# Kernel tuning notes

Hardware: AMD Instinct MI355X
Metric: run time of the kernel (lower is better)

The kernel has to match this reference:

```python
import jax, jax.numpy as jnp
import numpy as np

DM = 512; NH = 8; EL = 3; FACTOR = 3; EPS = 1e-5

def layernorm(x, g, b):
    m = x.mean(-1, keepdims=True)
    v = x.var(-1, keepdims=True)
    return (x - m) / jnp.sqrt(v + EPS) * g + b

def pos_embed(L, d):
    pos = jnp.arange(L, dtype=jnp.float32)[:, None]
    div = jnp.exp(jnp.arange(0, d, 2, dtype=jnp.float32) * (-np.log(10000.0) / d))
    pe = jnp.zeros((L, d), jnp.float32)
    pe = pe.at[:, 0::2].set(jnp.sin(pos * div))
    pe = pe.at[:, 1::2].set(jnp.cos(pos * div))
    return pe

def circ_conv1d(x, w, b=None):
    # x: [B,L,Cin], w: [Cout,Cin,3]; torch Conv1d padding=1, padding_mode='circular'
    xp = jnp.concatenate([x[:, -1:], x, x[:, :1]], axis=1)
    y = jax.lax.conv_general_dilated(xp, w, (1,), 'VALID', dimension_numbers=('NWC', 'OIW', 'NWC'))
    return y if b is None else y + b

def prob_attention(q, k, v, rng):
    # q,k,v: [B,H,L,D] -- Informer ProbSparse attention (non-masked encoder case)
    B, H, L, D = q.shape
    LK = k.shape[2]
    U = min(int(FACTOR * np.ceil(np.log(LK))), LK)   # sampled keys per query
    u = min(int(FACTOR * np.ceil(np.log(L))), L)     # top queries kept
    idx = jax.random.randint(rng, (L, U), 0, LK)     # shared across B,H as in torch
    k_samp = k[:, :, idx]                            # [B,H,L,U,D]
    qk = jnp.einsum('bhld,bhlud->bhlu', q, k_samp)
    M = qk.max(-1) - qk.sum(-1) / LK                 # sparsity measure
    top = jax.lax.top_k(M, u)[1]                     # [B,H,u]
    q_red = jnp.take_along_axis(q, top[..., None], axis=2)
    scores = jnp.einsum('bhud,bhkd->bhuk', q_red, k) / jnp.sqrt(jnp.asarray(D, q.dtype))
    attn = jax.nn.softmax(scores, axis=-1)
    upd = jnp.einsum('bhuk,bhkd->bhud', attn, v)
    ctx = jnp.broadcast_to(v.mean(axis=2, keepdims=True), (B, H, L, D))
    bi = jnp.arange(B)[:, None, None]
    hi = jnp.arange(H)[None, :, None]
    return ctx.at[bi, hi, top].set(upd)

def encoder_layer(x, p, rng):
    Wq_, bq_, Wk_, bk_, Wv_, bv_, Wo_, bo_, w1, b1, w2, b2, g1, be1, g2, be2 = p
    B, L, _ = x.shape
    D = DM // NH
    q = (x @ Wq_.T + bq_).reshape(B, L, NH, D).transpose(0, 2, 1, 3)
    k = (x @ Wk_.T + bk_).reshape(B, L, NH, D).transpose(0, 2, 1, 3)
    v = (x @ Wv_.T + bv_).reshape(B, L, NH, D).transpose(0, 2, 1, 3)
    ctx = prob_attention(q, k, v, rng).transpose(0, 2, 1, 3).reshape(B, L, DM)
    x = x + (ctx @ Wo_.T + bo_)
    x = layernorm(x, g1, be1)
    y = jax.nn.gelu(x @ w1.T + b1, approximate=False)  # pointwise conv1 (k=1)
    y = y @ w2.T + b2                                   # pointwise conv2 (k=1)
    return layernorm(x + y, g2, be2)

def distil_layer(x, w, b, g, beta):
    y = circ_conv1d(x, w, b)                 # Conv1d k=3 circular
    mu = y.mean((0, 1))
    var = y.var((0, 1))                      # BatchNorm1d, training stats
    y = (y - mu) / jnp.sqrt(var + EPS) * g + beta
    y = jax.nn.elu(y)
    # MaxPool1d(kernel=3, stride=2, padding=1)
    return jax.lax.reduce_window(y, -jnp.inf, jax.lax.max, (1, 3, 1), (1, 2, 1), ((0, 0), (1, 1), (0, 0)))

def setup_inputs():
    key = jax.random.key(0)
    ks = jax.random.split(key, 12)
    B, S, CIN, COUT, DFF = 8, 2048, 7, 7, 2048
    r = lambda k, s: jax.random.normal(k, s, jnp.float32)
    return {
        'x_enc': r(ks[0], (B, S, CIN)),
        'tok_w': r(ks[1], (DM, CIN, 3)) * (2.0 / (CIN * 3)) ** 0.5,
        'Wq': r(ks[2], (EL, DM, DM)) * DM ** -0.5, 'bq': jnp.zeros((EL, DM)),
        'Wk': r(ks[3], (EL, DM, DM)) * DM ** -0.5, 'bk': jnp.zeros((EL, DM)),
        'Wv': r(ks[4], (EL, DM, DM)) * DM ** -0.5, 'bv': jnp.zeros((EL, DM)),
        'Wo': r(ks[5], (EL, DM, DM)) * DM ** -0.5, 'bo': jnp.zeros((EL, DM)),
        'conv1_w': r(ks[6], (EL, DFF, DM)) * DM ** -0.5, 'conv1_b': jnp.zeros((EL, DFF)),
        'conv2_w': r(ks[7], (EL, DM, DFF)) * DFF ** -0.5, 'conv2_b': jnp.zeros((EL, DM)),
        'ln1_g': jnp.ones((EL, DM)), 'ln1_b': jnp.zeros((EL, DM)),
        'ln2_g': jnp.ones((EL, DM)), 'ln2_b': jnp.zeros((EL, DM)),
        'dconv_w': r(ks[8], (EL - 1, DM, DM, 3)) * (DM * 3) ** -0.5, 'dconv_b': jnp.zeros((EL - 1, DM)),
        'bn_g': jnp.ones((EL - 1, DM)), 'bn_b': jnp.zeros((EL - 1, DM)),
        'lnf_g': jnp.ones((DM,)), 'lnf_b': jnp.zeros((DM,)),
        'end_w': r(ks[9], (COUT, DM)) * DM ** -0.5, 'end_b': jnp.zeros((COUT,)),
    }

def reference(x_enc, tok_w, Wq, bq, Wk, bk, Wv, bv, Wo, bo, conv1_w, conv1_b, conv2_w, conv2_b, ln1_g, ln1_b, ln2_g, ln2_b, dconv_w, dconv_b, bn_g, bn_b, lnf_g, lnf_b, end_w, end_b):
    x = circ_conv1d(x_enc, tok_w) + pos_embed(x_enc.shape[1], DM)  # DataEmbedding
    base = jax.random.key(42)
    for l in range(EL):
        p = (Wq[l], bq[l], Wk[l], bk[l], Wv[l], bv[l], Wo[l], bo[l],
             conv1_w[l], conv1_b[l], conv2_w[l], conv2_b[l],
             ln1_g[l], ln1_b[l], ln2_g[l], ln2_b[l])
        x = encoder_layer(x, p, jax.random.fold_in(base, l))
        if l < EL - 1:
            x = distil_layer(x, dconv_w[l], dconv_b[l], bn_g[l], bn_b[l])
    x = layernorm(x, lnf_g, lnf_b)
    return x @ end_w.T + end_b  # end_conv2 (Conv1d k=1)
```

## Files before the change

### kernel.cpp

```cpp
#include <hip/hip_runtime.h>
#include <cstdint>
#include <cstddef>

#define DMODEL 512
#define NHEAD 8
#define HD 64

typedef _Float16 half8 __attribute__((ext_vector_type(8)));
typedef float f32x4 __attribute__((ext_vector_type(4)));

__device__ __forceinline__ uint32_t rotl32(uint32_t x, int r) {
  return (x << r) | (x >> (32 - r));
}

__device__ __forceinline__ void tf_block(uint32_t k0, uint32_t k1,
                                         uint32_t& x0, uint32_t& x1) {
  uint32_t ks0 = k0, ks1 = k1, ks2 = k0 ^ k1 ^ 0x1BD11BDAu;
  x0 += ks0; x1 += ks1;
  x0 += x1; x1 = rotl32(x1, 13); x1 ^= x0;
  x0 += x1; x1 = rotl32(x1, 15); x1 ^= x0;
  x0 += x1; x1 = rotl32(x1, 26); x1 ^= x0;
  x0 += x1; x1 = rotl32(x1, 6);  x1 ^= x0;
  x0 += ks1; x1 += ks2 + 1u;
  x0 += x1; x1 = rotl32(x1, 17); x1 ^= x0;
  x0 += x1; x1 = rotl32(x1, 29); x1 ^= x0;
  x0 += x1; x1 = rotl32(x1, 16); x1 ^= x0;
  x0 += x1; x1 = rotl32(x1, 24); x1 ^= x0;
  x0 += ks2; x1 += ks0 + 2u;
  x0 += x1; x1 = rotl32(x1, 13); x1 ^= x0;
  x0 += x1; x1 = rotl32(x1, 15); x1 ^= x0;
  x0 += x1; x1 = rotl32(x1, 26); x1 ^= x0;
  x0 += x1; x1 = rotl32(x1, 6);  x1 ^= x0;
  x0 += ks0; x1 += ks1 + 3u;
  x0 += x1; x1 = rotl32(x1, 17); x1 ^= x0;
  x0 += x1; x1 = rotl32(x1, 29); x1 ^= x0;
  x0 += x1; x1 = rotl32(x1, 16); x1 ^= x0;
  x0 += x1; x1 = rotl32(x1, 24); x1 ^= x0;
  x0 += ks1; x1 += ks2 + 4u;
  x0 += x1; x1 = rotl32(x1, 13); x1 ^= x0;
  x0 += x1; x1 = rotl32(x1, 15); x1 ^= x0;
  x0 += x1; x1 = rotl32(x1, 26); x1 ^= x0;
  x0 += x1; x1 = rotl32(x1, 6);  x1 ^= x0;
  x0 += ks2; x1 += ks0 + 5u;
}

__global__ void idx_kernel(int* __restrict__ idxb, int n, int layer, int mask) {
  int e = blockIdx.x * 256 + threadIdx.x;
  if (e >= n) return;
  uint32_t f0 = 0u, f1 = (uint32_t)layer;
  tf_block(0u, 42u, f0, f1);
  uint32_t s0 = 0u, s1 = 1u;
  tf_block(f0, f1, s0, s1);
  uint32_t x0 = 0u, x1 = (uint32_t)e;
  tf_block(s0, s1, x0, x1);
  uint32_t bits = x0 ^ x1;
  idxb[e] = (int)(bits & (uint32_t)mask);
}

__device__ __forceinline__ void f2hsplit(float v, unsigned short& h,
                                         unsigned short& l) {
  _Float16 hh = (_Float16)v;
  float r = v - (float)hh;
  _Float16 ll = (_Float16)r;
  h = __builtin_bit_cast(unsigned short, hh);
  l = __builtin_bit_cast(unsigned short, ll);
}

__device__ __forceinline__ float gelu_f(float v) {
  return 0.5f * v * (1.0f + erff(v * 0.7071067811865476f));
}

#define AS1G(p) ((const __attribute__((address_space(1))) void*)(size_t)(p))
#define AS3L(p) ((__attribute__((address_space(3))) void*)(unsigned)(size_t)(p))
#define GLD16(g, l) __builtin_amdgcn_global_load_lds(AS1G(g), AS3L(l), 16, 0, 0)

__global__ __launch_bounds__(256) void cvt_kernel(const float* __restrict__ X,
                                                  unsigned short* __restrict__ H,
                                                  unsigned short* __restrict__ Lo,
                                                  int n8) {
  int i = blockIdx.x * 256 + threadIdx.x;
  if (i >= n8) return;
  const float4* xp = (const float4*)X + 2 * (size_t)i;
  float4 a = xp[0], b = xp[1];
  float v[8] = {a.x, a.y, a.z, a.w, b.x, b.y, b.z, b.w};
  unsigned hu[4], lu[4];
#pragma unroll
  for (int q = 0; q < 4; ++q) {
    unsigned short h0, l0, h1, l1;
    f2hsplit(v[2 * q], h0, l0);
    f2hsplit(v[2 * q + 1], h1, l1);
    hu[q] = (unsigned)h0 | ((unsigned)h1 << 16);
    lu[q] = (unsigned)l0 | ((unsigned)l1 << 16);
  }
  uint4 hv; hv.x = hu[0]; hv.y = hu[1]; hv.z = hu[2]; hv.w = hu[3];
  uint4 lv; lv.x = lu[0]; lv.y = lu[1]; lv.z = lu[2]; lv.w = lu[3];
  *(uint4*)(H + 8 * (size_t)i) = hv;
  *(uint4*)(Lo + 8 * (size_t)i) = lv;
}

__global__ void packw2_kernel(const float* __restrict__ dw,
                              unsigned short* __restrict__ Hh,
                              unsigned short* __restrict__ Hl) {
  int gid = blockIdx.x * 256 + threadIdx.x;
  int o = gid / 1536;
  int kk = gid - o * 1536;
  int ww = kk / 512;
  int c = kk - ww * 512;
  float v = dw[((size_t)o * 512 + c) * 3 + ww];
  unsigned short h, l;
  f2hsplit(v, h, l);
  Hh[gid] = h;
  Hl[gid] = l;
}

template <int ACT, int HASR, int CONV, int F16OUT, int QKV, int PART>
__global__ __launch_bounds__(256, 4) void gemm_mfma(
    const unsigned short* __restrict__ Ah, const unsigned short* __restrict__ Al,
    const unsigned short* __restrict__ Wh, const unsigned short* __restrict__ Wl,
    const float* __restrict__ bias, const float* __restrict__ bias2,
    const float* __restrict__ bias3, const float* __restrict__ Rres,
    float* __restrict__ C, float* __restrict__ C2, float* __restrict__ C3,
    unsigned short* __restrict__ Ch, unsigned short* __restrict__ Cl,
    int N, int K, int Lmask, int ntx, int nty, int kloop) {
  __shared__ __attribute__((aligned(16))) unsigned short AsH[4096];
  __shared__ __attribute__((aligned(16))) unsigned short AsL[4096];
  __shared__ __attribute__((aligned(16))) unsigned short WsH[4096];
  __shared__ __attribute__((aligned(16))) unsigned short WsL[4096];
  const int tid = threadIdx.x;
  int blk = blockIdx.x;
  int kb = 0;
  if (PART) {
    const int tiles = ntx * nty;
    kb = blk / tiles;
    blk -= kb * tiles;
  }
  const int koff = PART ? kb * kloop : 0;
  const int xcd = blk & 7;
  const int j = blk >> 3;
  const int jr = j / ntx;
  const int row_t = xcd * (nty >> 3) + jr;
  const int col_t = j - jr * ntx;
  const int row0 = row_t << 7, col0 = col_t << 7;
  const int lane = tid & 63;
  const int wv = tid >> 6;
  const int wr = wv >> 1, wc = wv & 1;
  const int srow = lane >> 2;
  const int skoff = (((lane & 3) ^ ((lane >> 3) & 3)) << 3);
  const int l15 = lane & 15, lg = lane >> 4;
  const int slotx = ((lg ^ ((l15 >> 1) & 3)) << 4);
  int oa[4], ow[4];
#pragma unroll
  for (int t = 0; t < 4; ++t) {
    oa[t] = (((wr << 6) + (t << 4) + l15) << 6) + slotx;
    ow[t] = (((wc << 6) + (t << 4) + l15) << 6) + slotx;
  }
  f32x4 acc[4][4] = {};
  const int T = (PART ? kloop : K) >> 5;
  for (int it = 0; it < T; ++it) {
    const int k0 = koff + (it << 5);
    int wwin = 0, kc = k0;
    if (CONV) { wwin = k0 >> 9; kc = k0 & 511; }
#pragma unroll
    for (int g = 0; g < 2; ++g) {
      const int R0 = (wv << 5) + (g << 4);
      const int rr = R0 + srow;
      size_t aoff;
      if (CONV) {
        int t0 = row0 + rr;
        int tcv = t0 & Lmask, bb = t0 & ~Lmask;
        int src = bb | ((tcv - 1 + wwin) & Lmask);
        aoff = (size_t)src * 512 + (kc + skoff);
      } else {
        aoff = (size_t)(row0 + rr) * K + (k0 + skoff);
      }
      size_t woff = (size_t)(col0 + rr) * K + (k0 + skoff);
      GLD16(Ah + aoff, AsH + R0 * 32);
      GLD16(Al + aoff, AsL + R0 * 32);
      GLD16(Wh + woff, WsH + R0 * 32);
      GLD16(Wl + woff, WsL + R0 * 32);
    }
// ... 316 lines not shown
    const float* __restrict__ Q, const float* __restrict__ Kb,
    const int* __restrict__ idxb, float* __restrict__ Mout, int L, int U) {
  int i = blockIdx.x;
  int b = i & 7;
  int j = i >> 3;
  int chunks = L >> 8;
  int h = j / chunks;
  int c = j - h * chunks;
  int t = c * 256 + threadIdx.x;
  const float4* qr = (const float4*)(Q + ((size_t)(b * L + t)) * DMODEL + h * HD);
  float4 qv[16];
#pragma unroll
  for (int ii = 0; ii < 16; ii++) qv[ii] = qr[ii];
  float mx = -3.4e38f, sm = 0.f;
  for (int jj = 0; jj < U; jj++) {
    int kr = idxb[t * U + jj];
    const float4* kp =
        (const float4*)(Kb + ((size_t)(b * L + kr)) * DMODEL + h * HD);
    float dot = 0.f;
#pragma unroll
    for (int ii = 0; ii < 16; ii++) {
      float4 kv = kp[ii];
      dot += qv[ii].x * kv.x + qv[ii].y * kv.y + qv[ii].z * kv.z + qv[ii].w * kv.w;
    }
    mx = fmaxf(mx, dot);
    sm += dot;
  }
  Mout[(size_t)(b * 8 + h) * L + t] = mx - sm / (float)L;
}

__global__ __launch_bounds__(256) void topk_kernel(const float* __restrict__ Mv,
                                                   int* __restrict__ topb, int L,
                                                   int u) {
  __shared__ float wv_s[4];
  __shared__ int wi_s[4];
  __shared__ int best_s;
  int bh = blockIdx.x, tid = threadIdx.x;
  int lane = tid & 63, w = tid >> 6;
  int cnt = L >> 8;
  float lv[8];
  for (int i = 0; i < cnt; i++) lv[i] = Mv[(size_t)bh * L + i * 256 + tid];
  for (int r = 0; r < u; r++) {
    float bv = -3.4e38f;
    int bi = 0x7fffffff;
    for (int i = 0; i < cnt; i++) {
      if (lv[i] > bv) { bv = lv[i]; bi = i * 256 + tid; }
    }
    for (int s = 32; s > 0; s >>= 1) {
      float ov = __shfl_down(bv, s);
      int oi = __shfl_down(bi, s);
      if (ov > bv || (ov == bv && oi < bi)) { bv = ov; bi = oi; }
    }
    if (lane == 0) { wv_s[w] = bv; wi_s[w] = bi; }
    __syncthreads();
    if (tid == 0) {
      float fv = wv_s[0];
      int fi = wi_s[0];
      for (int q = 1; q < 4; q++) {
        if (wv_s[q] > fv || (wv_s[q] == fv && wi_s[q] < fi)) {
          fv = wv_s[q];
          fi = wi_s[q];
        }
      }
      best_s = fi;
      topb[bh * u + r] = fi;
    }
    __syncthreads();
    int win = best_s;
    if ((win & 255) == tid) lv[win >> 8] = -3.4e38f;
  }
}

__global__ void gatherq_kernel(const float* __restrict__ Q,
                               const int* __restrict__ topb,
                               float* __restrict__ qsel, int L, int u) {
  int i = blockIdx.x;
  int bh = i / u;
  int b = bh >> 3, h = bh & 7;
  int t = topb[i];
  qsel[i * HD + threadIdx.x] =
      Q[((size_t)(b * L + t)) * DMODEL + h * HD + threadIdx.x];
}

__global__ __launch_bounds__(256) void xmean_kernel(const float* __restrict__ x,
                                                    float* __restrict__ psumx,
                                                    int L) {
  int i = blockIdx.x;
  int b = i >> 3, g = i & 7;
  int rows = L >> 3;
  int tid = threadIdx.x;
  const float* base = x + ((size_t)b * L + (size_t)g * rows) * DMODEL;
  float s0 = 0.f, s1 = 0.f;
  for (int t = 0; t < rows; t++) {
    s0 += base[(size_t)t * DMODEL + tid];
    s1 += base[(size_t)t * DMODEL + tid + 256];
  }
  psumx[i * DMODEL + tid] = s0;
  psumx[i * DMODEL + tid + 256] = s1;
}

__global__ __launch_bounds__(256) void mvmake_kernel(
    const float* __restrict__ psumx, const float* __restrict__ Wv,
    const float* __restrict__ bv, const float* __restrict__ Wo,
    const float* __restrict__ bo, float* __restrict__ mvg,
    float* __restrict__ mvWog, int L) {
  __shared__ float xm[512];
  __shared__ float mvs[512];
  int b = blockIdx.x, tid = threadIdx.x;
  float inv = 1.0f / (float)L;
  for (int nn = 0; nn < 2; nn++) {
    int c = tid + nn * 256;
    float s = 0.f;
    for (int g = 0; g < 8; g++) s += psumx[(b * 8 + g) * DMODEL + c];
    xm[c] = s * inv;
  }
  __syncthreads();
  for (int nn = 0; nn < 2; nn++) {
    int n = tid + nn * 256;
    const float* wr = Wv + (size_t)n * 512;
    float s = bv[n];
    for (int k = 0; k < 512; k += 4) {
      float4 w4 = *(const float4*)(wr + k);
      s += xm[k] * w4.x + xm[k + 1] * w4.y + xm[k + 2] * w4.z + xm[k + 3] * w4.w;
    }
    mvs[n] = s;
    mvg[b * DMODEL + n] = s;
  }
  __syncthreads();
  for (int nn = 0; nn < 2; nn++) {
    int n = tid + nn * 256;
    const float* wr = Wo + (size_t)n * 512;
    float s = bo[n];
    for (int k = 0; k < 512; k += 4) {
      float4 w4 = *(const float4*)(wr + k);
      s += mvs[k] * w4.x + mvs[k + 1] * w4.y + mvs[k + 2] * w4.z +
           mvs[k + 3] * w4.w;
    }
    mvWog[b * DMODEL + n] = s;
  }
}

__global__ void x1bcast_kernel(const float* __restrict__ x,
                               const float* __restrict__ mvWog,
                               float* __restrict__ x1, int L) {
  int gid = blockIdx.x * 256 + threadIdx.x;
  int c = gid & 511;
  int r = gid >> 9;
  int b = r / L;
  x1[gid] = x[gid] + mvWog[b * DMODEL + c];
}

template <int GQ>
__global__ __launch_bounds__(256) void attnflash_kernel(
    const float* __restrict__ qsrc, const int* __restrict__ topb,
    const float* __restrict__ Kb, const float* __restrict__ Vb,
    float* __restrict__ pm, float* __restrict__ pl, float* __restrict__ pO,
    int L, int u, int nchunk) {
  __shared__ float qs[24][64];
  __shared__ float Kt[64][68];
  __shared__ float Ps[24][68];
  int blk = blockIdx.x;
  int bh = blk / nchunk;
  int c = blk - bh * nchunk;
  int b = bh >> 3, h = bh & 7;
  int cs = L / nchunk;
  int tid = threadIdx.x;
  int lane = tid & 63;
  int w = tid >> 6;
  if (GQ) {
    for (int i = tid; i < u * 64; i += 256) {
      int r = i >> 6, d = i & 63;
      int t = topb[bh * u + r];
      qs[r][d] = qsrc[((size_t)(b * L + t)) * DMODEL + h * HD + d];
    }
  } else {
    for (int i = tid; i < u * 64; i += 256)
      qs[i >> 6][i & 63] = qsrc[(size_t)bh * u * 64 + i];
  }
  float m[6], l[6], O[6];
#pragma unroll
  for (int k = 0; k < 6; k++) { m[k] = -3.4e38f; l[k] = 0.f; O[k] = 0.f; }
// ... 197 lines not shown
    unsigned short h, l;
    f2hsplit(y0, h, l);
    Hh[gbase + tid] = h;
    Hl[gbase + tid] = l;
    f2hsplit(y1, h, l);
    Hh[gbase + tid + 256] = h;
    Hl[gbase + tid + 256] = l;
  } else {
    Y[gbase + tid] = y0;
    Y[gbase + tid + 256] = y1;
  }
}

__global__ __launch_bounds__(256) void bnpart_kernel(const float* __restrict__ z,
                                                     float* __restrict__ psum,
                                                     float* __restrict__ psq,
                                                     int rowsPer) {
  int blk = blockIdx.x, tid = threadIdx.x;
  size_t r0 = (size_t)blk * rowsPer;
  float s0 = 0, q0 = 0, s1 = 0, q1 = 0;
  for (int r = 0; r < rowsPer; r++) {
    const float* zp = z + (r0 + r) * DMODEL;
    float a = zp[tid];
    s0 += a; q0 += a * a;
    float c = zp[tid + 256];
    s1 += c; q1 += c * c;
  }
  psum[blk * DMODEL + tid] = s0;
  psum[blk * DMODEL + tid + 256] = s1;
  psq[blk * DMODEL + tid] = q0;
  psq[blk * DMODEL + tid + 256] = q1;
}

__global__ void bnfin_kernel(const float* __restrict__ psum,
                             const float* __restrict__ psq, float* __restrict__ mu,
                             float* __restrict__ var, int nb, int Rtot) {
  int c = blockIdx.x * 256 + threadIdx.x;
  float s = 0, q = 0;
  for (int b = 0; b < nb; b++) {
    s += psum[b * DMODEL + c];
    q += psq[b * DMODEL + c];
  }
  float m = s / (float)Rtot;
  mu[c] = m;
  var[c] = fmaxf(q / (float)Rtot - m * m, 0.f);
}

template <int EMIT>
__global__ void bnpool_kernel(const float* __restrict__ z,
                              const float* __restrict__ mu,
                              const float* __restrict__ var,
                              const float* __restrict__ g,
                              const float* __restrict__ bta,
                              float* __restrict__ out,
                              unsigned short* __restrict__ Hh,
                              unsigned short* __restrict__ Hl, int L) {
  int gid = blockIdx.x * 256 + threadIdx.x;
  int c = gid & 511;
  int bt = gid >> 9;
  int L2 = L >> 1;
  int t2 = bt % L2, b = bt / L2;
  float m = mu[c];
  float inv = 1.0f / sqrtf(var[c] + 1e-5f);
  float gg = g[c], bb = bta[c];
  float best = -3.4e38f;
#pragma unroll
  for (int ww = 0; ww < 3; ww++) {
    int t = 2 * t2 - 1 + ww;
    if (t < 0 || t >= L) continue;
    float yv = (z[((size_t)(b * L + t)) * DMODEL + c] - m) * inv * gg + bb;
    yv = (yv > 0.f) ? yv : expm1f(yv);
    best = fmaxf(best, yv);
  }
  out[gid] = best;
  if (EMIT) {
    unsigned short h, l;
    f2hsplit(best, h, l);
    Hh[gid] = h;
    Hl[gid] = l;
  }
}

__global__ __launch_bounds__(64) void end_kernel(const float* __restrict__ xn,
                                                 const float* __restrict__ ew,
                                                 const float* __restrict__ eb,
                                                 float* __restrict__ out) {
  __shared__ float xs[512];
  __shared__ float red[64];
  int row = blockIdx.x, tid = threadIdx.x;
#pragma unroll
  for (int i = 0; i < 8; i++) xs[tid + 64 * i] = xn[(size_t)row * DMODEL + tid + 64 * i];
  __syncthreads();
  for (int c = 0; c < 7; c++) {
    float p = 0.f;
    for (int d = tid; d < 512; d += 64) p += xs[d] * ew[c * DMODEL + d];
    red[tid] = p;
    __syncthreads();
    for (int s = 32; s > 0; s >>= 1) {
      if (tid < s) red[tid] += red[tid + s];
      __syncthreads();
    }
    if (tid == 0) out[row * 7 + c] = red[0] + eb[c];
    __syncthreads();
  }
}

extern "C" void kernel_launch(void* const* d_in, const int* in_sizes, int n_in,
                              void* d_out, int out_size, void* d_ws,
                              size_t ws_size, hipStream_t stream) {
  (void)in_sizes; (void)n_in; (void)out_size;
  const float* x_enc = (const float*)d_in[0];
  const float* tok_w = (const float*)d_in[1];
  const float* Wq = (const float*)d_in[2];
  const float* bq = (const float*)d_in[3];
  const float* Wk = (const float*)d_in[4];
  const float* bk = (const float*)d_in[5];
  const float* Wv = (const float*)d_in[6];
  const float* bv = (const float*)d_in[7];
  const float* Wo = (const float*)d_in[8];
  const float* bo = (const float*)d_in[9];
  const float* w1 = (const float*)d_in[10];
  const float* b1 = (const float*)d_in[11];
  const float* w2 = (const float*)d_in[12];
  const float* b2 = (const float*)d_in[13];
  const float* g1 = (const float*)d_in[14];
  const float* be1 = (const float*)d_in[15];
  const float* g2 = (const float*)d_in[16];
  const float* be2 = (const float*)d_in[17];
  const float* dw = (const float*)d_in[18];
  const float* db = (const float*)d_in[19];
  const float* bng = (const float*)d_in[20];
  const float* bnb = (const float*)d_in[21];
  const float* lnfg = (const float*)d_in[22];
  const float* lnfb = (const float*)d_in[23];
  const float* endw = (const float*)d_in[24];
  const float* endb = (const float*)d_in[25];
  float* out = (float*)d_out;
  char* ws = (char*)d_ws;

  const int B = 8;
  const int S = 2048;
  const int Uarr[3] = {24, 21, 21};
  const int NCHMAX = 32;

  size_t o = 0;
  float* buf0 = (float*)(ws + o); o += (size_t)16384 * 512 * 4;
  float* qbuf = (float*)(ws + o); o += (size_t)16384 * 512 * 4;
  float* kbuf = (float*)(ws + o); o += (size_t)16384 * 512 * 4;
  float* Mb    = (float*)(ws + o); o += (size_t)64 * 2048 * 4;
  int*   idxb  = (int*)(ws + o);   o += (size_t)2048 * 24 * 4;
  int*   topb  = (int*)(ws + o);   o += 8192;
  float* qsel  = (float*)(ws + o); o += (size_t)64 * 24 * 64 * 4;
  float* mvg   = (float*)(ws + o); o += (size_t)8 * 512 * 4;
  float* mvWog = (float*)(ws + o); o += (size_t)8 * 512 * 4;
  float* psumx = (float*)(ws + o); o += (size_t)64 * 512 * 4;
  float* psum  = (float*)(ws + o); o += (size_t)128 * 512 * 4;
  float* psq   = (float*)(ws + o); o += (size_t)128 * 512 * 4;
  float* muv   = (float*)(ws + o); o += 2048;
  float* varv  = (float*)(ws + o); o += 2048;
  float* pmb   = (float*)(ws + o); o += (size_t)64 * NCHMAX * 24 * 4;
  float* plb   = (float*)(ws + o); o += (size_t)64 * NCHMAX * 24 * 4;
  float* pOb   = (float*)(ws + o); o += (size_t)64 * NCHMAX * 24 * 64 * 4;
  unsigned short* P1h = (unsigned short*)(ws + o); o += (size_t)16384 * 512 * 2;
  unsigned short* P1l = (unsigned short*)(ws + o); o += (size_t)16384 * 512 * 2;
  unsigned short* P2h = (unsigned short*)(ws + o); o += (size_t)16384 * 512 * 2;
  unsigned short* P2l = (unsigned short*)(ws + o); o += (size_t)16384 * 512 * 2;
  unsigned short* Wqkvh = (unsigned short*)(ws + o); o += (size_t)1536 * 512 * 2;
  unsigned short* Wqkvl = (unsigned short*)(ws + o); o += (size_t)1536 * 512 * 2;
  unsigned short* w1h = (unsigned short*)(ws + o); o += (size_t)2048 * 512 * 2;
  unsigned short* w1l = (unsigned short*)(ws + o); o += (size_t)2048 * 512 * 2;
  unsigned short* w2h = (unsigned short*)(ws + o); o += (size_t)512 * 2048 * 2;
  unsigned short* w2l = (unsigned short*)(ws + o); o += (size_t)512 * 2048 * 2;
  unsigned short* wph = (unsigned short*)(ws + o); o += (size_t)512 * 1536 * 2;
  unsigned short* wpl = (unsigned short*)(ws + o); o += (size_t)512 * 1536 * 2;
  const bool use_mfma = (ws_size >= o);
  float* vbuf = (float*)(ws + o); o += (size_t)16384 * 512 * 4;
  const bool fuseqkv = (ws_size >= o);
  unsigned short* CHh = (unsigned short*)(ws + o); o += (size_t)16384 * 2048 * 2;
  unsigned short* CHl = (unsigned short*)(ws + o); o += (size_t)16384 * 2048 * 2;
  const bool fullffn = (ws_size >= o);
  unsigned short* CHb0 = (unsigned short*)buf0;
  float* partmP1 = (float*)P1h;
  float* petab = (float*)pOb;

  if (use_mfma) {
    petab_kernel<<<S * DMODEL / 256, 256, 0, stream>>>(petab, S);
    tokpe_kernel<1, 1><<<B * S * DMODEL / 256, 256, 0, stream>>>(
        x_enc, tok_w, petab, buf0, P1h, P1l, S);
    int L = S;
    for (int l = 0; l < 3; l++) {
      int U = Uarr[l];
      int u = Uarr[l];
      int BL = B * L;
      int nty = BL >> 7;
      int nch = L >> 6;
      if (nch > NCHMAX) nch = NCHMAX;
      cvt_kernel<<<128, 256, 0, stream>>>(Wq + (size_t)l * 262144, Wqkvh, Wqkvl, 32768);
      cvt_kernel<<<128, 256, 0, stream>>>(Wk + (size_t)l * 262144, Wqkvh + 262144,
                                          Wqkvl + 262144, 32768);
      cvt_kernel<<<128, 256, 0, stream>>>(Wv + (size_t)l * 262144, Wqkvh + 524288,
                                          Wqkvl + 524288, 32768);
      if (fuseqkv) {
        gemm_mfma<0, 0, 0, 0, 1, 0><<<12 * nty, 256, 0, stream>>>(
            P1h, P1l, Wqkvh, Wqkvl, bq + l * 512, bk + l * 512, bv + l * 512,
            nullptr, qbuf, kbuf, vbuf, nullptr, nullptr, 1536, 512, 0, 12, nty,
            512);
      } else {
        idx_kernel<<<(L * U + 255) / 256, 256, 0, stream>>>(idxb, L * U, l, L - 1);
        gemm_mfma<0, 0, 0, 0, 0, 0><<<4 * nty, 256, 0, stream>>>(
            P1h, P1l, Wqkvh, Wqkvl, bq + l * 512, nullptr, nullptr, nullptr,
            qbuf, nullptr, nullptr, nullptr, nullptr, 512, 512, 0, 4, nty, 512);
        gemm_mfma<0, 0, 0, 0, 0, 0><<<4 * nty, 256, 0, stream>>>(
            P1h, P1l, Wqkvh + 262144, Wqkvl + 262144, bk + l * 512, nullptr,
            nullptr, nullptr, kbuf, nullptr, nullptr, nullptr, nullptr, 512,
            512, 0, 4, nty, 512);
      }
      mscore4_kernel<<<64 * (L >> 6), 256, 0, stream>>>(qbuf, kbuf, Mb, L, U, l);
      topk_kernel<<<64, 256, 0, stream>>>(Mb, topb, L, u);
      xmean_kernel<<<64, 256, 0, stream>>>(buf0, psumx, L);
      mvmake_kernel<<<8, 256, 0, stream>>>(psumx, Wv + (size_t)l * 262144,
                                           bv + l * 512, Wo + (size_t)l * 262144,
                                           bo + l * 512, mvg, mvWog, L);
      if (fuseqkv) {
        attnflash_kernel<1><<<64 * nch, 256, 0, stream>>>(
            qbuf, topb, kbuf, vbuf, pmb, plb, pOb, L, u, nch);
      } else {
        gatherq_kernel<<<64 * u, 64, 0, stream>>>(qbuf, topb, qsel, L, u);
        gemm_mfma<0, 0, 0, 0, 0, 0><<<4 * nty, 256, 0, stream>>>(
            P1h, P1l, Wqkvh + 524288, Wqkvl + 524288, bv + l * 512, nullptr,
            nullptr, nullptr, qbuf, nullptr, nullptr, nullptr, nullptr, 512,
            512, 0, 4, nty, 512);
        attnflash_kernel<0><<<64 * nch, 256, 0, stream>>>(
            qsel, nullptr, kbuf, qbuf, pmb, plb, pOb, L, u, nch);
      }
      deltaWo_kernel<<<64 * u, 256, 0, stream>>>(pmb, plb, pOb, mvg, topb,
                                                 Wo + (size_t)l * 262144, buf0, L,
                                                 u, nch);
      ln_kernel<1, 1><<<BL, 256, 0, stream>>>(buf0, g1 + l * 512, be1 + l * 512,
                                              qbuf, P2h, P2l, mvWog, L);
      cvt_kernel<<<512, 256, 0, stream>>>(w1 + (size_t)l * 1048576, w1h, w1l, 131072);
      cvt_kernel<<<512, 256, 0, stream>>>(w2 + (size_t)l * 1048576, w2h, w2l, 131072);
      if (fullffn) {
        gemm_mfma<1, 0, 0, 1, 0, 0><<<16 * nty, 256, 0, stream>>>(
            P2h, P2l, w1h, w1l, b1 + l * 2048, nullptr, nullptr, nullptr,
            nullptr, nullptr, nullptr, CHh, CHl, 2048, 512, 0, 16, nty, 512);
        gemm_mfma<0, 1, 0, 0, 0, 0><<<4 * nty, 256, 0, stream>>>(
            CHh, CHl, w2h, w2l, b2 + l * 512, nullptr, nullptr, qbuf, kbuf,
            nullptr, nullptr, nullptr, nullptr, 512, 2048, 0, 4, nty, 2048);
        if (l < 2) {
          ln_kernel<1, 0><<<BL, 256, 0, stream>>>(kbuf, g2 + l * 512,
                                                  be2 + l * 512, buf0, P1h, P1l,
                                                  nullptr, 1);
        } else {
          ln_kernel<0, 0><<<BL, 256, 0, stream>>>(kbuf, g2 + l * 512,
                                                  be2 + l * 512, buf0, nullptr,
                                                  nullptr, nullptr, 1);
        }
      } else if (fuseqkv) {
        if (l < 2) {
          const int R = 8192;
          const int Rt = R >> 7;
          unsigned short* CHhp = (unsigned short*)vbuf;
          unsigned short* CHlp = (unsigned short*)kbuf;
          float* partp = buf0;
          for (int r0 = 0; r0 < BL; r0 += R) {
            gemm_mfma<1, 0, 0, 1, 0, 0><<<16 * Rt, 256, 0, stream>>>(
                P2h + (size_t)r0 * 512, P2l + (size_t)r0 * 512, w1h, w1l,
                b1 + l * 2048, nullptr, nullptr, nullptr, nullptr, nullptr,
                nullptr, CHhp, CHlp, 2048, 512, 0, 16, Rt, 512);
            gemm_mfma<0, 0, 0, 0, 0, 1><<<4 * Rt * 2, 256, 0, stream>>>(
                CHhp, CHlp, w2h, w2l, nullptr, nullptr, nullptr, nullptr, partp,
                nullptr, nullptr, nullptr, nullptr, 512, 2048, 0, 4, Rt, 1024);
            lncomb_kernel<1><<<R, 256, 0, stream>>>(
                partp, b2 + l * 512, qbuf, g2 + l * 512, be2 + l * 512, nullptr,
                P1h, P1l, r0, (size_t)R * 512, 2);
          }
        } else {
          unsigned short* CHhp = (unsigned short*)vbuf;
          unsigned short* CHlp = CHhp + (size_t)4096 * 2048;
          gemm_mfma<1, 0, 0, 1, 0, 0><<<16 * 32, 256, 0, stream>>>(
              P2h, P2l, w1h, w1l, b1 + l * 2048, nullptr, nullptr, nullptr,
              nullptr, nullptr, nullptr, CHhp, CHlp, 2048, 512, 0, 16, 32, 512);
          gemm_mfma<0, 0, 0, 0, 0, 1><<<4 * 32 * 4, 256, 0, stream>>>(
              CHhp, CHlp, w2h, w2l, nullptr, nullptr, nullptr, nullptr, kbuf,
              nullptr, nullptr, nullptr, nullptr, 512, 2048, 0, 4, 32, 512);
          lncomb_kernel<0><<<4096, 256, 0, stream>>>(
              kbuf, b2 + l * 512, qbuf, g2 + l * 512, be2 + l * 512, buf0,
              nullptr, nullptr, 0, (size_t)4096 * 512, 4);
        }
      } else {
        unsigned short* CHlch = CHb0 + (size_t)4096 * 2048;
        for (int r0 = 0; r0 < BL; r0 += 4096) {
          gemm_mfma<1, 0, 0, 1, 0, 0><<<16 * 32, 256, 0, stream>>>(
              P2h + (size_t)r0 * 512, P2l + (size_t)r0 * 512, w1h, w1l,
              b1 + l * 2048, nullptr, nullptr, nullptr, nullptr, nullptr,
              nullptr, CHb0, CHlch, 2048, 512, 0, 16, 32, 512);
          gemm_mfma<0, 0, 0, 0, 0, 1><<<4 * 32 * 4, 256, 0, stream>>>(
              CHb0, CHlch, w2h, w2l, nullptr, nullptr, nullptr, nullptr,
              partmP1, nullptr, nullptr, nullptr, nullptr, 512, 2048, 0, 4, 32,
              512);
          combine_kernel<1><<<4096 * 512 / 256, 256, 0, stream>>>(
              partmP1, b2 + l * 512, qbuf + (size_t)r0 * 512,
              kbuf + (size_t)r0 * 512, (size_t)4096 * 512, 4);
        }
        if (l < 2) {
          ln_kernel<1, 0><<<BL, 256, 0, stream>>>(kbuf, g2 + l * 512,
                                                  be2 + l * 512, buf0, P1h, P1l,
                                                  nullptr, 1);
        } else {
          ln_kernel<0, 0><<<BL, 256, 0, stream>>>(kbuf, g2 + l * 512,
                                                  be2 + l * 512, buf0, nullptr,
                                                  nullptr, nullptr, 1);
        }
      }
      if (l < 2) {
        packw2_kernel<<<512 * 1536 / 256, 256, 0, stream>>>(
            dw + (size_t)l * 512 * 512 * 3, wph, wpl);
        gemm_mfma<0, 0, 1, 0, 0, 0><<<4 * nty, 256, 0, stream>>>(
            P1h, P1l, wph, wpl, db + l * 512, nullptr, nullptr, nullptr, kbuf,
            nullptr, nullptr, nullptr, nullptr, 512, 1536, L - 1, 4, nty, 1536);
        int nb = BL / 128;
        bnpart_kernel<<<nb, 256, 0, stream>>>(kbuf, psum, psq, 128);
        bnfin_kernel<<<2, 256, 0, stream>>>(psum, psq, muv, varv, nb, BL);
        bnpool_kernel<1><<<(BL / 2) * 512 / 256, 256, 0, stream>>>(
            kbuf, muv, varv, bng + l * 512, bnb + l * 512, buf0, P1h, P1l, L);
        L >>= 1;
      }
    }
    int BL = B * L;
    ln_kernel<0, 0><<<BL, 256, 0, stream>>>(buf0, lnfg, lnfb, qbuf, nullptr,
                                            nullptr, nullptr, 1);
    end_kernel<<<BL, 64, 0, stream>>>(qbuf, endw, endb, out);
    return;
  }

  {
    const int NCH = 8;
    size_t o2 = 0;
    float* buf0f = (float*)(ws + o2); o2 += (size_t)16384 * 512 * 4;
    float* qbuff = (float*)(ws + o2); o2 += (size_t)16384 * 512 * 4;
    float* kbuff = (float*)(ws + o2); o2 += (size_t)16384 * 512 * 4;
    float* wpack = (float*)(ws + o2); o2 += (size_t)512 * 1536 * 4;
    float* Mbf    = (float*)(ws + o2); o2 += (size_t)64 * 2048 * 4;
    int*   idxbf  = (int*)(ws + o2);   o2 += (size_t)2048 * 24 * 4;
    int*   topbf  = (int*)(ws + o2);   o2 += 8192;
    float* qself  = (float*)(ws + o2); o2 += (size_t)64 * 24 * 64 * 4;
    float* mvgf   = (float*)(ws + o2); o2 += (size_t)8 * 512 * 4;
    float* mvWogf = (float*)(ws + o2); o2 += (size_t)8 * 512 * 4;
    float* psumxf = (float*)(ws + o2); o2 += (size_t)64 * 512 * 4;
    float* psumf  = (float*)(ws + o2); o2 += (size_t)128 * 512 * 4;
    float* psqf   = (float*)(ws + o2); o2 += (size_t)128 * 512 * 4;
    float* muvf   = (float*)(ws + o2); o2 += 2048;
    float* varvf  = (float*)(ws + o2); o2 += 2048;
    float* pmbf   = (float*)(ws + o2); o2 += (size_t)64 * NCH * 24 * 4;
    float* plbf   = (float*)(ws + o2); o2 += (size_t)64 * NCH * 24 * 4;
    float* pObf   = (float*)(ws + o2); o2 += (size_t)64 * NCH * 24 * 64 * 4;
    float* partb  = (float*)(ws + o2); o2 += (size_t)4 * 4096 * 2048;
    const bool uks = (ws_size >= o2);

    tokpe_kernel<0, 0><<<B * S * DMODEL / 256, 256, 0, stream>>>(
        x_enc, tok_w, nullptr, buf0f, nullptr, nullptr, S);
    int L = S;
    for (int l = 0; l < 3; l++) {
      int U = Uarr[l];
      int u = U;
      int BL = B * L;
      int nty = BL / 128;
      size_t MN = (size_t)BL * 512;
      int gq = 4 * nty;
      int ksq = (gq >= 512 || !uks) ? 1 : (512 / gq);
      idx_kernel<<<(L * U + 255) / 256, 256, 0, stream>>>(idxbf, L * U, l, L - 1);
      if (ksq == 1) {
        gemm128<0, 0, 0, 0><<<gq, 256, 0, stream>>>(
            buf0f, Wq + (size_t)l * 262144, bq + l * 512, nullptr, qbuff, 512,
            512, 0, 4, nty, 512, 1);
        gemm128<0, 0, 0, 0><<<gq, 256, 0, stream>>>(
            buf0f, Wk + (size_t)l * 262144, bk + l * 512, nullptr, kbuff, 512,
            512, 0, 4, nty, 512, 1);
      } else {
        gemm128<0, 0, 0, 1><<<gq * ksq, 256, 0, stream>>>(
            buf0f, Wq + (size_t)l * 262144, nullptr, nullptr, partb, 512, 512, 0,
            4, nty, 512 / ksq, ksq);
        combine_kernel<0><<<(unsigned)(MN / 256), 256, 0, stream>>>(
            partb, bq + l * 512, nullptr, qbuff, MN, ksq);
        gemm128<0, 0, 0, 1><<<gq * ksq, 256, 0, stream>>>(
            buf0f, Wk + (size_t)l * 262144, nullptr, nullptr, partb, 512, 512, 0,
            4, nty, 512 / ksq, ksq);
        combine_kernel<0><<<(unsigned)(MN / 256), 256, 0, stream>>>(
            partb, bk + l * 512, nullptr, kbuff, MN, ksq);
      }
      mscore_kernel<<<8 * 8 * L / 256, 256, 0, stream>>>(qbuff, kbuff, idxbf, Mbf, L, U);
      topk_kernel<<<64, 256, 0, stream>>>(Mbf, topbf, L, u);
      gatherq_kernel<<<64 * u, 64, 0, stream>>>(qbuff, topbf, qself, L, u);
      xmean_kernel<<<64, 256, 0, stream>>>(buf0f, psumxf, L);
      mvmake_kernel<<<8, 256, 0, stream>>>(psumxf, Wv + (size_t)l * 262144,
                                           bv + l * 512, Wo + (size_t)l * 262144,
                                           bo + l * 512, mvgf, mvWogf, L);
      if (ksq == 1) {
        gemm128<0, 0, 0, 0><<<gq, 256, 0, stream>>>(
            buf0f, Wv + (size_t)l * 262144, bv + l * 512, nullptr, qbuff, 512,
            512, 0, 4, nty, 512, 1);
      } else {
        gemm128<0, 0, 0, 1><<<gq * ksq, 256, 0, stream>>>(
            buf0f, Wv + (size_t)l * 262144, nullptr, nullptr, partb, 512, 512, 0,
            4, nty, 512 / ksq, ksq);
        combine_kernel<0><<<(unsigned)(MN / 256), 256, 0, stream>>>(
            partb, bv + l * 512, nullptr, qbuff, MN, ksq);
      }
      attnflash_kernel<0><<<64 * NCH, 256, 0, stream>>>(
          qself, nullptr, kbuff, qbuff, pmbf, plbf, pObf, L, u, NCH);
      x1bcast_kernel<<<(unsigned)(MN / 256), 256, 0, stream>>>(buf0f, mvWogf, kbuff, L);
      deltaWo_kernel<<<64 * u, 256, 0, stream>>>(pmbf, plbf, pObf, mvgf, topbf,
                                                 Wo + (size_t)l * 262144, kbuff,
                                                 L, u, NCH);
      ln_kernel<0, 0><<<BL, 256, 0, stream>>>(kbuff, g1 + l * 512, be1 + l * 512,
                                              qbuff, nullptr, nullptr, nullptr, 1);
      for (int r0 = 0; r0 < BL; r0 += 4096) {
        gemm128<1, 0, 0, 0><<<16 * 32, 256, 0, stream>>>(
            qbuff + (size_t)r0 * 512, w1 + (size_t)l * 2048 * 512, b1 + l * 2048,
            nullptr, buf0f, 2048, 512, 0, 16, 32, 512, 1);
        if (uks) {
          gemm128<0, 0, 0, 1><<<4 * 32 * 4, 256, 0, stream>>>(
              buf0f, w2 + (size_t)l * 512 * 2048, nullptr, nullptr, partb, 512,
              2048, 0, 4, 32, 512, 4);
          combine_kernel<1><<<4096 * 512 / 256, 256, 0, stream>>>(
              partb, b2 + l * 512, qbuff + (size_t)r0 * 512,
              kbuff + (size_t)r0 * 512, (size_t)4096 * 512, 4);
        } else {
          gemm128<0, 1, 0, 0><<<4 * 32, 256, 0, stream>>>(
              buf0f, w2 + (size_t)l * 512 * 2048, b2 + l * 512,
              qbuff + (size_t)r0 * 512, kbuff + (size_t)r0 * 512, 512, 2048, 0,
              4, 32, 2048, 1);
        }
      }
      ln_kernel<0, 0><<<BL, 256, 0, stream>>>(kbuff, g2 + l * 512, be2 + l * 512,
                                              buf0f, nullptr, nullptr, nullptr, 1);

      if (l < 2) {
        packw_kernel<<<512 * 1536 / 256, 256, 0, stream>>>(
            dw + (size_t)l * 512 * 512 * 3, wpack);
        int ksc = (gq >= 512 || !uks) ? 1 : 2;
        if (ksc == 1) {
          gemm128<0, 0, 1, 0><<<gq, 256, 0, stream>>>(
              buf0f, wpack, db + l * 512, nullptr, kbuff, 512, 1536, L - 1, 4,
              nty, 1536, 1);
        } else {
          gemm128<0, 0, 1, 1><<<gq * 2, 256, 0, stream>>>(
              buf0f, wpack, nullptr, nullptr, partb, 512, 1536, L - 1, 4, nty,
              768, 2);
          combine_kernel<0><<<(unsigned)(MN / 256), 256, 0, stream>>>(
              partb, db + l * 512, nullptr, kbuff, MN, 2);
        }
        int nb = BL / 128;
        bnpart_kernel<<<nb, 256, 0, stream>>>(kbuff, psumf, psqf, 128);
        bnfin_kernel<<<2, 256, 0, stream>>>(psumf, psqf, muvf, varvf, nb, BL);
        bnpool_kernel<0><<<(BL / 2) * 512 / 256, 256, 0, stream>>>(
            kbuff, muvf, varvf, bng + l * 512, bnb + l * 512, buf0f, nullptr,
            nullptr, L);
        L >>= 1;
      }
    }
    int BL = B * L;
    ln_kernel<0, 0><<<BL, 256, 0, stream>>>(buf0f, lnfg, lnfb, qbuff, nullptr,
                                            nullptr, nullptr, 1);
    end_kernel<<<BL, 64, 0, stream>>>(qbuff, endw, endb, out);
  }
}
```

Before: 1.966 ms.

## Batch weight conversions, parallelize mean-V path, fuse final layernorm into end kernel

```diff
diff --git a/kernel.cpp b/kernel.cpp
--- a/kernel.cpp
+++ b/kernel.cpp
@@ -74,28 +74,63 @@
 #define AS3L(p) ((__attribute__((address_space(3))) void*)(unsigned)(size_t)(p))
 #define GLD16(g, l) __builtin_amdgcn_global_load_lds(AS1G(g), AS3L(l), 16, 0, 0)
 
+__device__ __forceinline__ void cvt_body(const float* __restrict__ X,
+                                         unsigned short* __restrict__ H,
+                                         unsigned short* __restrict__ Lo,
+                                         int i) {
+  const float4* xp = (const float4*)X + 2 * (size_t)i;
+  float4 a = xp[0], b = xp[1];
+  float v[8] = {a.x, a.y, a.z, a.w, b.x, b.y, b.z, b.w};
+  unsigned hu[4], lu[4];
+#pragma unroll
+  for (int q = 0; q < 4; ++q) {
+    unsigned short h0, l0, h1, l1;
+    f2hsplit(v[2 * q], h0, l0);
+    f2hsplit(v[2 * q + 1], h1, l1);
+    hu[q] = (unsigned)h0 | ((unsigned)h1 << 16);
+    lu[q] = (unsigned)l0 | ((unsigned)l1 << 16);
+  }
+  uint4 hv; hv.x = hu[0]; hv.y = hu[1]; hv.z = hu[2]; hv.w = hu[3];
+  uint4 lv; lv.x = lu[0]; lv.y = lu[1]; lv.z = lu[2]; lv.w = lu[3];
+  *(uint4*)(H + 8 * (size_t)i) = hv;
+  *(uint4*)(Lo + 8 * (size_t)i) = lv;
+}
+
 __global__ __launch_bounds__(256) void cvt_kernel(const float* __restrict__ X,
                                                   unsigned short* __restrict__ H,
                                                   unsigned short* __restrict__ Lo,
                                                   int n8) {
   int i = blockIdx.x * 256 + threadIdx.x;
   if (i >= n8) return;
-  const float4* xp = (const float4*)X + 2 * (size_t)i;
-  float4 a = xp[0], b = xp[1];
-  float v[8] = {a.x, a.y, a.z, a.w, b.x, b.y, b.z, b.w};
-  unsigned hu[4], lu[4];
-#pragma unroll
-  for (int q = 0; q < 4; ++q) {
-    unsigned short h0, l0, h1, l1;
-    f2hsplit(v[2 * q], h0, l0);
-    f2hsplit(v[2 * q + 1], h1, l1);
-    hu[q] = (unsigned)h0 | ((unsigned)h1 << 16);
-    lu[q] = (unsigned)l0 | ((unsigned)l1 << 16);
-  }
-  uint4 hv; hv.x = hu[0]; hv.y = hu[1]; hv.z = hu[2]; hv.w = hu[3];
-  uint4 lv; lv.x = lu[0]; lv.y = lu[1]; lv.z = lu[2]; lv.w = lu[3];
-  *(uint4*)(H + 8 * (size_t)i) = hv;
-  *(uint4*)(Lo + 8 * (size_t)i) = lv;
+  cvt_body(X, H, Lo, i);
+}
+
+__global__ __launch_bounds__(256) void cvt5_kernel(
+    const float* __restrict__ Wq, const float* __restrict__ Wk,
+    const float* __restrict__ Wv, const float* __restrict__ w1,
+    const float* __restrict__ w2, unsigned short* __restrict__ Qh,
+    unsigned short* __restrict__ Ql, unsigned short* __restrict__ w1h,
+    unsigned short* __restrict__ w1l, unsigned short* __restrict__ w2h,
+    unsigned short* __restrict__ w2l) {
+  int blk = blockIdx.x;
+  const float* src;
+  unsigned short* H;
+  unsigned short* Lo;
+  int lb;
+  if (blk < 384) {
+    int wsel = blk >> 7;
+    lb = blk & 127;
+    src = (wsel == 0) ? Wq : (wsel == 1 ? Wk : Wv);
+    H = Qh + (size_t)wsel * 262144;
+    Lo = Ql + (size_t)wsel * 262144;
+  } else if (blk < 896) {
+    lb = blk - 384;
+    src = w1; H = w1h; Lo = w1l;
+  } else {
+    lb = blk - 896;
+    src = w2; H = w2h; Lo = w2l;
+  }
+  cvt_body(src, H, Lo, lb * 256 + threadIdx.x);
 }
 
 __global__ void packw2_kernel(const float* __restrict__ dw,
@@ -578,6 +613,23 @@
       Q[((size_t)(b * L + t)) * DMODEL + h * HD + threadIdx.x];
 }
 
+__global__ __launch_bounds__(256) void xmean32_kernel(const float* __restrict__ x,
+                                                      float* __restrict__ psumx,
+                                                      int L) {
+  int i = blockIdx.x;
+  int b = i >> 5, g = i & 31;
+  int rows = L >> 5;
+  int tid = threadIdx.x;
+  const float* base = x + ((size_t)b * L + (size_t)g * rows) * DMODEL;
+  float s0 = 0.f, s1 = 0.f;
+  for (int t = 0; t < rows; t++) {
+    s0 += base[(size_t)t * DMODEL + tid];
+    s1 += base[(size_t)t * DMODEL + tid + 256];
+  }
+  psumx[i * DMODEL + tid] = s0;
+  psumx[i * DMODEL + tid + 256] = s1;
+}
+
 __global__ __launch_bounds__(256) void xmean_kernel(const float* __restrict__ x,
                                                     float* __restrict__ psumx,
                                                     int L) {
@@ -593,6 +645,59 @@
   }
   psumx[i * DMODEL + tid] = s0;
   psumx[i * DMODEL + tid + 256] = s1;
+}
+
+__global__ __launch_bounds__(256) void mvmake1_kernel(
+    const float* __restrict__ psumx, const float* __restrict__ Wv,
+    const float* __restrict__ bv, float* __restrict__ mvg, int L, int ng) {
+  __shared__ float xm[512];
+  int blk = blockIdx.x;
+  int b = blk >> 3, grp = blk & 7;
+  int tid = threadIdx.x;
+  float inv = 1.0f / (float)L;
+  for (int nn = 0; nn < 2; nn++) {
+    int c = tid + nn * 256;
+    float s = 0.f;
+    for (int g = 0; g < ng; g++) s += psumx[(b * ng + g) * DMODEL + c];
+    xm[c] = s * inv;
+  }
+  __syncthreads();
+  int n = grp * 64 + (tid >> 2);
+  int sub = tid & 3;
+  const float* wr = Wv + (size_t)n * 512 + sub * 128;
+  const float* xp = xm + sub * 128;
+  float s = 0.f;
+  for (int k = 0; k < 128; k += 4) {
+    float4 w4 = *(const float4*)(wr + k);
+    s += xp[k] * w4.x + xp[k + 1] * w4.y + xp[k + 2] * w4.z + xp[k + 3] * w4.w;
+  }
+  s += __shfl_xor(s, 1);
+  s += __shfl_xor(s, 2);
+  if (sub == 0) mvg[b * DMODEL + n] = s + bv[n];
+}
+
+__global__ __launch_bounds__(256) void mvmake2_kernel(
+    const float* __restrict__ mvg, const float* __restrict__ Wo,
+    const float* __restrict__ bo, float* __restrict__ mvWog) {
+  __shared__ float mv[512];
+  int blk = blockIdx.x;
+  int b = blk >> 3, grp = blk & 7;
+  int tid = threadIdx.x;
+  mv[tid] = mvg[b * DMODEL + tid];
+  mv[tid + 256] = mvg[b * DMODEL + tid + 256];
+  __syncthreads();
+  int n = grp * 64 + (tid >> 2);
+  int sub = tid & 3;
+  const float* wr = Wo + (size_t)n * 512 + sub * 128;
+  const float* xp = mv + sub * 128;
+  float s = 0.f;
+  for (int k = 0; k < 128; k += 4) {
+    float4 w4 = *(const float4*)(wr + k);
+    s += xp[k] * w4.x + xp[k + 1] * w4.y + xp[k + 2] * w4.z + xp[k + 3] * w4.w;
+  }
+  s += __shfl_xor(s, 1);
+  s += __shfl_xor(s, 2);
+  if (sub == 0) mvWog[b * DMODEL + n] = s + bo[n];
 }
 
 __global__ __launch_bounds__(256) void mvmake_kernel(
@@ -956,22 +1061,56 @@
 }
 
 __global__ __launch_bounds__(64) void end_kernel(const float* __restrict__ xn,
+                                                 const float* __restrict__ lg,
+                                                 const float* __restrict__ lb,
                                                  const float* __restrict__ ew,
                                                  const float* __restrict__ eb,
                                                  float* __restrict__ out) {
   __shared__ float xs[512];
   __shared__ float red[64];
   int row = blockIdx.x, tid = threadIdx.x;
-#pragma unroll
-  for (int i = 0; i < 8; i++) xs[tid + 64 * i] = xn[(size_t)row * DMODEL + tid + 64 * i];
+  float s = 0.f;
+#pragma unroll
+  for (int i = 0; i < 8; i++) {
+    float x = xn[(size_t)row * DMODEL + tid + 64 * i];
+    xs[tid + 64 * i] = x;
+    s += x;
+  }
+  red[tid] = s;
+  __syncthreads();
+  for (int st = 32; st > 0; st >>= 1) {
+    if (tid < st) red[tid] += red[tid + st];
+    __syncthreads();
+  }
+  float mean = red[0] * (1.0f / 512.0f);
+  __syncthreads();
+  float q = 0.f;
+#pragma unroll
+  for (int i = 0; i < 8; i++) {
+    float d = xs[tid + 64 * i] - mean;
+    q += d * d;
+  }
+  red[tid] = q;
+  __syncthreads();
+  for (int st = 32; st > 0; st >>= 1) {
+    if (tid < st) red[tid] += red[tid + st];
+    __syncthreads();
+  }
+  float inv = 1.0f / sqrtf(red[0] * (1.0f / 512.0f) + 1e-5f);
+  __syncthreads();
+#pragma unroll
+  for (int i = 0; i < 8; i++) {
+    int c = tid + 64 * i;
+    xs[c] = (xs[c] - mean) * inv * lg[c] + lb[c];
+  }
   __syncthreads();
   for (int c = 0; c < 7; c++) {
     float p = 0.f;
     for (int d = tid; d < 512; d += 64) p += xs[d] * ew[c * DMODEL + d];
     red[tid] = p;
     __syncthreads();
-    for (int s = 32; s > 0; s >>= 1) {
-      if (tid < s) red[tid] += red[tid + s];
+    for (int st = 32; st > 0; st >>= 1) {
+      if (tid < st) red[tid] += red[tid + st];
       __syncthreads();
     }
     if (tid == 0) out[row * 7 + c] = red[0] + eb[c];
@@ -1027,7 +1166,7 @@
   float* qsel  = (float*)(ws + o); o += (size_t)64 * 24 * 64 * 4;
   float* mvg   = (float*)(ws + o); o += (size_t)8 * 512 * 4;
   float* mvWog = (float*)(ws + o); o += (size_t)8 * 512 * 4;
-  float* psumx = (float*)(ws + o); o += (size_t)64 * 512 * 4;
+  float* psumx = (float*)(ws + o); o += (size_t)256 * 512 * 4;
   float* psum  = (float*)(ws + o); o += (size_t)128 * 512 * 4;
   float* psq   = (float*)(ws + o); o += (size_t)128 * 512 * 4;
   float* muv   = (float*)(ws + o); o += 2048;
@@ -1069,11 +1208,10 @@
       int nty = BL >> 7;
       int nch = L >> 6;
       if (nch > NCHMAX) nch = NCHMAX;
-      cvt_kernel<<<128, 256, 0, stream>>>(Wq + (size_t)l * 262144, Wqkvh, Wqkvl, 32768);
-      cvt_kernel<<<128, 256, 0, stream>>>(Wk + (size_t)l * 262144, Wqkvh + 262144,
-                                          Wqkvl + 262144, 32768);
-      cvt_kernel<<<128, 256, 0, stream>>>(Wv + (size_t)l * 262144, Wqkvh + 524288,
-                                          Wqkvl + 524288, 32768);
+      cvt5_kernel<<<1408, 256, 0, stream>>>(
+          Wq + (size_t)l * 262144, Wk + (size_t)l * 262144,
+          Wv + (size_t)l * 262144, w1 + (size_t)l * 1048576,
+          w2 + (size_t)l * 1048576, Wqkvh, Wqkvl, w1h, w1l, w2h, w2l);
       if (fuseqkv) {
         gemm_mfma<0, 0, 0, 0, 1, 0><<<12 * nty, 256, 0, stream>>>(
             P1h, P1l, Wqkvh, Wqkvl, bq + l * 512, bk + l * 512, bv + l * 512,
@@ -1091,10 +1229,11 @@
       }
       mscore4_kernel<<<64 * (L >> 6), 256, 0, stream>>>(qbuf, kbuf, Mb, L, U, l);
       topk_kernel<<<64, 256, 0, stream>>>(Mb, topb, L, u);
-      xmean_kernel<<<64, 256, 0, stream>>>(buf0, psumx, L);
-      mvmake_kernel<<<8, 256, 0, stream>>>(psumx, Wv + (size_t)l * 262144,
-                                           bv + l * 512, Wo + (size_t)l * 262144,
-                                           bo + l * 512, mvg, mvWog, L);
+      xmean32_kernel<<<256, 256, 0, stream>>>(buf0, psumx, L);
+      mvmake1_kernel<<<64, 256, 0, stream>>>(psumx, Wv + (size_t)l * 262144,
+                                             bv + l * 512, mvg, L, 32);
+      mvmake2_kernel<<<64, 256, 0, stream>>>(mvg, Wo + (size_t)l * 262144,
+                                             bo + l * 512, mvWog);
       if (fuseqkv) {
         attnflash_kernel<1><<<64 * nch, 256, 0, stream>>>(
             qbuf, topb, kbuf, vbuf, pmb, plb, pOb, L, u, nch);
@@ -1112,8 +1251,6 @@
                                                  u, nch);
       ln_kernel<1, 1><<<BL, 256, 0, stream>>>(buf0, g1 + l * 512, be1 + l * 512,
                                               qbuf, P2h, P2l, mvWog, L);
-      cvt_kernel<<<512, 256, 0, stream>>>(w1 + (size_t)l * 1048576, w1h, w1l, 131072);
-      cvt_kernel<<<512, 256, 0, stream>>>(w2 + (size_t)l * 1048576, w2h, w2l, 131072);
       if (fullffn) {
         gemm_mfma<1, 0, 0, 1, 0, 0><<<16 * nty, 256, 0, stream>>>(
             P2h, P2l, w1h, w1l, b1 + l * 2048, nullptr, nullptr, nullptr,
@@ -1202,9 +1339,7 @@
       }
     }
     int BL = B * L;
-    ln_kernel<0, 0><<<BL, 256, 0, stream>>>(buf0, lnfg, lnfb, qbuf, nullptr,
-                                            nullptr, nullptr, 1);
-    end_kernel<<<BL, 64, 0, stream>>>(qbuf, endw, endb, out);
+    end_kernel<<<BL, 64, 0, stream>>>(buf0, lnfg, lnfb, endw, endb, out);
     return;
   }
 
@@ -1335,8 +1470,6 @@
       }
     }
     int BL = B * L;
-    ln_kernel<0, 0><<<BL, 256, 0, stream>>>(buf0f, lnfg, lnfb, qbuff, nullptr,
-                                            nullptr, nullptr, 1);
-    end_kernel<<<BL, 64, 0, stream>>>(qbuff, endw, endb, out);
-  }
-}
+    end_kernel<<<BL, 64, 0, stream>>>(buf0f, lnfg, lnfb, endw, endb, out);
+  }
+}
```

Measured after the change: 1.780 ms. 1.1x faster.
